# Kernel optimization log

Hardware: AMD Instinct MI355X
Metric: run time of the kernel (lower is better)

## Reference

```python
import jax, jax.numpy as jnp
import numpy as np


def setup_inputs() -> dict:
    key = jax.random.key(0)
    k1, k2 = jax.random.split(key)
    B, G, N, C = 32, 64, 32, 3  # batch, num point groups, points per group, xyz
    xyz1_matrix = jax.random.normal(k1, (B, G, N, C), dtype=jnp.float32)
    xyz2_matrix = jax.random.normal(k2, (B, G, N, C), dtype=jnp.float32)
    return {"xyz1_matrix": xyz1_matrix, "xyz2_matrix": xyz2_matrix}


def reference(xyz1_matrix, xyz2_matrix):
    # xyz1_matrix: [B, G1, N1, 3], xyz2_matrix: [B, G2, N2, 3]
    # Pairwise squared L2 distances between every point of every group in set 1
    x2 = jnp.sum(xyz1_matrix * xyz1_matrix, axis=-1)  # [B, G1, N1]
    y2 = jnp.sum(xyz2_matrix * xyz2_matrix, axis=-1)  # [B, G2, N2]
    cross = jnp.einsum('bgnc,bhmc->bghnm', xyz1_matrix, xyz2_matrix)  # [B,G1,G2,N1,N2]
    d = x2[:, :, None, :, None] + y2[:, None, :, None, :] - 2.0 * cross
    # Nearest-neighbor (min over the other cloud) for both directions.
    dist1 = jnp.min(d, axis=-1)  # [B, G1, G2, N1]: for each pt in group g1, nearest in g2
    dist2 = jnp.min(d, axis=-2)  # [B, G1, G2, N2]: for each pt in group g2, nearest in g1
    # (dist2 here already corresponds to the torch dist2.permute(0, 2, 1, 3).)
    return jnp.mean(dist1, axis=-1) + jnp.mean(dist2, axis=-1)  # [B, G1, G2]
```

## Files before the change

### kernel.cpp

```cpp
#include <hip/hip_runtime.h>
#include <hip/hip_bf16.h>


__global__ __launch_bounds__(256, 2)
void chamfer_dist_kernel(const float* __restrict__ xyz1,
                         const float* __restrict__ xyz2,
                         float* __restrict__ out) {
    const int b    = blockIdx.x >> 4;
    const int g1   = ((blockIdx.x & 15) << 2) | (threadIdx.x >> 6);
    const int g2   = threadIdx.x & 63;

    const float* __restrict__ p2 = xyz2 + (size_t)(b * 64 + g2) * 96;
    float qx[32], qy[32], qz[32], s2[32];
#pragma unroll
    for (int m = 0; m < 32; ++m) {
        const float x = p2[3 * m + 0];
        const float y = p2[3 * m + 1];
        const float z = p2[3 * m + 2];
        s2[m] = fmaf(x, x, fmaf(y, y, z * z));
        qx[m] = -2.0f * x;
        qy[m] = -2.0f * y;
        qz[m] = -2.0f * z;
    }

    float colmin[32];
#pragma unroll
    for (int m = 0; m < 32; ++m) colmin[m] = 3.0e38f;

    const float* __restrict__ p1 = xyz1 + (size_t)(b * 64 + g1) * 96;
    float sum1 = 0.0f;

#pragma unroll 4
    for (int n = 0; n < 32; ++n) {
        const float x1 = p1[3 * n + 0];
        const float y1 = p1[3 * n + 1];
        const float z1 = p1[3 * n + 2];
        const float s1 = fmaf(x1, x1, fmaf(y1, y1, z1 * z1));
        float rmin = 3.0e38f;
#pragma unroll
        for (int m = 0; m < 32; ++m) {
            const float u = s1 + s2[m];
            const float t = fmaf(x1, qx[m], fmaf(y1, qy[m], fmaf(z1, qz[m], u)));
            rmin      = fminf(rmin, t);
            colmin[m] = fminf(colmin[m], t);
        }
        sum1 += rmin;
    }

    float sum2 = 0.0f;
#pragma unroll
    for (int m = 0; m < 32; ++m) sum2 += colmin[m];

    out[(size_t)(b * 64 + g1) * 64 + g2] = (sum1 + sum2) * (1.0f / 32.0f);
}

extern "C" void kernel_launch(void* const* d_in, const int* in_sizes, int n_in,
                              void* d_out, int out_size, void* d_ws, size_t ws_size,
                              hipStream_t stream) {
    const float* xyz1 = (const float*)d_in[0];
    const float* xyz2 = (const float*)d_in[1];
    float* out = (float*)d_out;

    dim3 grid(512);
    dim3 block(256);
    chamfer_dist_kernel<<<grid, block, 0, stream>>>(xyz1, xyz2, out);
}
```

Baseline: 72.63 us.

## Split each group pair across two half-wave lanes and combine via shuffles

Each (g1,g2) pair is now handled by two lanes, each owning 16 of the 32 points of group g2. Row minima and column sums are combined across the wave halves with __shfl_xor. The grid doubles to 1024 blocks and launch bounds rise to 4 blocks per CU, cutting per-thread registers to raise occupancy. xyz2 is loaded with float4 vector loads. The cost is extra shuffles, a reduction tree, and half the lanes doing redundant stores that are masked off.

```diff
diff --git a/kernel.cpp b/kernel.cpp
--- a/kernel.cpp
+++ b/kernel.cpp
@@ -2,56 +2,81 @@
 #include <hip/hip_bf16.h>
 
 
-__global__ __launch_bounds__(256, 2)
+__global__ __launch_bounds__(256, 4)
 void chamfer_dist_kernel(const float* __restrict__ xyz1,
                          const float* __restrict__ xyz2,
                          float* __restrict__ out) {
-    const int b    = blockIdx.x >> 4;
-    const int g1   = ((blockIdx.x & 15) << 2) | (threadIdx.x >> 6);
-    const int g2   = threadIdx.x & 63;
+    const int tid  = threadIdx.x;
+    const int w    = tid >> 6;
+    const int lane = tid & 63;
+    const int mh   = lane >> 5;
+    const int b    = blockIdx.x >> 5;
+    const int g1   = ((blockIdx.x & 31) << 1) | (w >> 1);
+    const int g2   = ((w & 1) << 5) | (lane & 31);
 
-    const float* __restrict__ p2 = xyz2 + (size_t)(b * 64 + g2) * 96;
-    float qx[32], qy[32], qz[32], s2[32];
+    const float4* __restrict__ p2v =
+        (const float4*)(xyz2 + (size_t)(b * 64 + g2) * 96 + mh * 48);
+    float buf[48];
 #pragma unroll
-    for (int m = 0; m < 32; ++m) {
-        const float x = p2[3 * m + 0];
-        const float y = p2[3 * m + 1];
-        const float z = p2[3 * m + 2];
-        s2[m] = fmaf(x, x, fmaf(y, y, z * z));
-        qx[m] = -2.0f * x;
-        qy[m] = -2.0f * y;
-        qz[m] = -2.0f * z;
+    for (int i = 0; i < 12; ++i) {
+        const float4 v = p2v[i];
+        buf[4 * i + 0] = v.x;
+        buf[4 * i + 1] = v.y;
+        buf[4 * i + 2] = v.z;
+        buf[4 * i + 3] = v.w;
+    }
+    float x2[16], y2[16], z2[16], s2[16];
+#pragma unroll
+    for (int j = 0; j < 16; ++j) {
+        x2[j] = buf[3 * j + 0];
+        y2[j] = buf[3 * j + 1];
+        z2[j] = buf[3 * j + 2];
+        s2[j] = fmaf(x2[j], x2[j], fmaf(y2[j], y2[j], z2[j] * z2[j]));
     }
 
-    float colmin[32];
+    float colmin[16];
 #pragma unroll
-    for (int m = 0; m < 32; ++m) colmin[m] = 3.0e38f;
+    for (int j = 0; j < 16; ++j) colmin[j] = 3.0e38f;
 
     const float* __restrict__ p1 = xyz1 + (size_t)(b * 64 + g1) * 96;
     float sum1 = 0.0f;
 
-#pragma unroll 4
+#pragma unroll 2
     for (int n = 0; n < 32; ++n) {
         const float x1 = p1[3 * n + 0];
         const float y1 = p1[3 * n + 1];
         const float z1 = p1[3 * n + 2];
         const float s1 = fmaf(x1, x1, fmaf(y1, y1, z1 * z1));
-        float rmin = 3.0e38f;
+        const float a = -2.0f * x1;
+        const float c = -2.0f * y1;
+        const float e = -2.0f * z1;
+
+        float t[16];
 #pragma unroll
-        for (int m = 0; m < 32; ++m) {
-            const float u = s1 + s2[m];
-            const float t = fmaf(x1, qx[m], fmaf(y1, qy[m], fmaf(z1, qz[m], u)));
-            rmin      = fminf(rmin, t);
-            colmin[m] = fminf(colmin[m], t);
+        for (int j = 0; j < 16; ++j) {
+            t[j] = fmaf(a, x2[j], fmaf(c, y2[j], fmaf(e, z2[j], s1 + s2[j])));
+            colmin[j] = fminf(colmin[j], t[j]);
         }
-        sum1 += rmin;
+#pragma unroll
+        for (int s = 8; s > 0; s >>= 1) {
+#pragma unroll
+            for (int j = 0; j < s; ++j) t[j] = fminf(t[j], t[j + s]);
+        }
+        const float other = __shfl_xor(t[0], 32, 64);
+        sum1 += fminf(t[0], other);
     }
 
-    float sum2 = 0.0f;
 #pragma unroll
-    for (int m = 0; m < 32; ++m) sum2 += colmin[m];
+    for (int s = 8; s > 0; s >>= 1) {
+#pragma unroll
+        for (int j = 0; j < s; ++j) colmin[j] += colmin[j + s];
+    }
+    const float sum2 = colmin[0] + __shfl_xor(colmin[0], 32, 64);
 
-    out[(size_t)(b * 64 + g1) * 64 + g2] = (sum1 + sum2) * (1.0f / 32.0f);
+    const float res = (sum1 + sum2) * (1.0f / 32.0f);
+    if (mh == 0) {
+        out[(size_t)(b * 64 + g1) * 64 + g2] = res;
+    }
 }
 
 extern "C" void kernel_launch(void* const* d_in, const int* in_sizes, int n_in,
@@ -61,7 +86,7 @@
     const float* xyz2 = (const float*)d_in[1];
     float* out = (float*)d_out;
 
-    dim3 grid(512);
+    dim3 grid(1024);
     dim3 block(256);
     chamfer_dist_kernel<<<grid, block, 0, stream>>>(xyz1, xyz2, out);
 }
```

After: 74.21 us. 2.2% more time.
